# Performance work log

Hardware: AMD Instinct MI355X
Metric: run time of the kernel (lower is better)

Reference implementation:

```python
import jax, jax.numpy as jnp
import numpy as np

GAMMA = 2.5
K = 4
RHO = 0.085
TAU_CLIP = 5.0
NUM_HEADS = 8


def setup_inputs() -> dict:
    key = jax.random.key(0)
    ks = jax.random.split(key, 4)
    B, T, C = 2, 2048, 512
    x = jax.random.normal(ks[0], (B, T, C), jnp.float32)
    tau = jax.random.uniform(ks[1], (B, T, T), jnp.float32)
    s = 1.0 / np.sqrt(C)
    Wqkv = jax.random.normal(ks[2], (C, 3 * C), jnp.float32) * s
    bqkv = jnp.zeros((3 * C,), jnp.float32)
    Wproj = jax.random.normal(ks[3], (C, C), jnp.float32) * s
    bproj = jnp.zeros((C,), jnp.float32)
    return dict(x=x, tau=tau, Wqkv=Wqkv, bqkv=bqkv, Wproj=Wproj, bproj=bproj)


def reference(x, tau, Wqkv, bqkv, Wproj, bproj):
    B, T, C = x.shape
    H = NUM_HEADS
    D = C // H
    qkv = x @ Wqkv + bqkv                       # [B,T,3C]
    q, k, v = jnp.split(qkv, 3, axis=-1)
    q = q.reshape(B, T, H, D).transpose(0, 2, 1, 3)   # [B,H,T,D]
    k = k.reshape(B, T, H, D).transpose(0, 2, 1, 3)
    v = v.reshape(B, T, H, D).transpose(0, 2, 1, 3)
    scale = D ** -0.5
    logits = jnp.einsum('bhtd,bhsd->bhts', q, k) * scale   # [B,H,T,T]
    pheromone_bias = GAMMA * jnp.log(tau + 1e-8)           # [B,T,T]
    logits = logits + pheromone_bias[:, None]
    # top-K keys per query from tau define the sparse mask (LOCAL_WINDOW=0)
    k_val = min(K, T)
    idx = jax.lax.top_k(tau, k_val)[1]                     # [B,T,K]
    mask = jnp.zeros((B, T, T), bool).at[
        jnp.arange(B)[:, None, None], jnp.arange(T)[None, :, None], idx
    ].set(True)
    logits = jnp.where(mask[:, None], logits, -jnp.inf)
    attn = jax.nn.softmax(logits, axis=-1)                 # [B,H,T,T]
    # EMA pheromone (tau) update, no gradient in original (torch.no_grad)
    signal = attn.mean(axis=1)                             # [B,T,T]
    tau_new = (1.0 - RHO) * tau + signal ** 3
    tau_new = tau_new / (tau_new.sum(axis=-1, keepdims=True) + 1e-8)
    tau_new = jnp.minimum(tau_new, TAU_CLIP)
    tau_new = jax.lax.stop_gradient(tau_new)
    out = jnp.einsum('bhts,bhsd->bthd', attn, v).reshape(B, T, C)
    out = out @ Wproj + bproj
    return out, tau_new
```

## Files before the change

kernel.cpp:

```cpp
#include <hip/hip_runtime.h>
#include <hip/hip_bf16.h>
#include <math.h>

#define BB 2
#define TT 2048
#define CC 512
#define HH 8
#define DD 64
#define KK 4
#define C3 1536
#define MROWS (BB*TT)

#define G1_NT (C3/64)
#define G1_BLOCKS (G1_NT*(MROWS/128))
#define G2_NT (CC/64)
#define G2_BLOCKS (G2_NT*(MROWS/64))

typedef __attribute__((ext_vector_type(8))) short bf16x8;
typedef __attribute__((ext_vector_type(4))) float floatx4;

static __device__ __forceinline__ unsigned short f2bf(float f) {
  unsigned int u = __float_as_uint(f);
  return (unsigned short)((u + 0x7fffu + ((u >> 16) & 1u)) >> 16);
}
static __device__ __forceinline__ float bf2f(unsigned short u) {
  return __uint_as_float(((unsigned int)u) << 16);
}

static __device__ __forceinline__ int xcd_swz(int bid, int nblk) {
  const int cpx = nblk >> 3;
  return (bid & 7) * cpx + (bid >> 3);
}

template<bool BF16OUT>
static __device__ __forceinline__ void gemm_body(
    int bid, int nt,
    const unsigned short* __restrict__ A,
    const unsigned short* __restrict__ Bt,
    const float* __restrict__ bias,
    void* __restrict__ Cout, int N, int K) {
  __shared__ unsigned short As[128][64];
  __shared__ unsigned short Bs[64][64];
  const int tid  = threadIdx.x;
  const int wave = tid >> 6;
  const int lane = tid & 63;
  const int n0 = (bid % nt) * 64;
  const int m0 = (bid / nt) * 128;
  const int m_off = (wave >> 1) * 64;
  const int n_off = (wave & 1) * 32;
  const int fr = lane & 15;
  const int fq = lane >> 4;
  const int srow   = lane >> 3;
  const int schunk = ((lane & 7) ^ srow) * 8;

  floatx4 acc[4][2];
#pragma unroll
  for (int i = 0; i < 4; ++i)
#pragma unroll
    for (int j = 0; j < 2; ++j) acc[i][j] = (floatx4){0.f, 0.f, 0.f, 0.f};

  for (int k0 = 0; k0 < K; k0 += 64) {
#pragma unroll
    for (int s = 0; s < 4; ++s) {
      const int r0 = wave * 32 + s * 8;
      const unsigned short* ga = A + (size_t)(m0 + r0 + srow) * K + k0 + schunk;
      __builtin_amdgcn_global_load_lds(
          (const __attribute__((address_space(1))) void*)ga,
          (__attribute__((address_space(3))) void*)&As[r0][0], 16, 0, 0);
    }
#pragma unroll
    for (int s = 0; s < 2; ++s) {
      const int r0 = wave * 16 + s * 8;
      const unsigned short* gb = Bt + (size_t)(n0 + r0 + srow) * K + k0 + schunk;
      __builtin_amdgcn_global_load_lds(
          (const __attribute__((address_space(1))) void*)gb,
          (__attribute__((address_space(3))) void*)&Bs[r0][0], 16, 0, 0);
    }
    __syncthreads();
#pragma unroll
    for (int kk = 0; kk < 2; ++kk) {
      bf16x8 a[4], b[2];
#pragma unroll
      for (int i = 0; i < 4; ++i) {
        const int row = m_off + i * 16 + fr;
        a[i] = *(const bf16x8*)&As[row][(((kk << 2) + fq) ^ (row & 7)) * 8];
      }
#pragma unroll
      for (int j = 0; j < 2; ++j) {
        const int row = n_off + j * 16 + fr;
        b[j] = *(const bf16x8*)&Bs[row][(((kk << 2) + fq) ^ (row & 7)) * 8];
      }
#pragma unroll
      for (int i = 0; i < 4; ++i)
#pragma unroll
        for (int j = 0; j < 2; ++j)
          acc[i][j] = __builtin_amdgcn_mfma_f32_16x16x32_bf16(a[i], b[j], acc[i][j], 0, 0, 0);
    }
    __syncthreads();
  }
#pragma unroll
  for (int j = 0; j < 2; ++j) {
    int col = n0 + n_off + j * 16 + fr;
    float bv = bias[col];
#pragma unroll
    for (int i = 0; i < 4; ++i) {
#pragma unroll
      for (int r = 0; r < 4; ++r) {
        int row = m0 + m_off + i * 16 + fq * 4 + r;
        float v = acc[i][j][r] + bv;
        if (BF16OUT) ((unsigned short*)Cout)[(size_t)row * N + col] = f2bf(v);
        else         ((float*)Cout)[(size_t)row * N + col] = v;
      }
    }
  }
}

static __device__ __forceinline__ void gemm_body64(
    int bid, int nt,
    const unsigned short* __restrict__ A,
    const unsigned short* __restrict__ Bt,
    const float* __restrict__ bias,
    float* __restrict__ Cout, int N, int K) {
  __shared__ unsigned short As[64][64];
  __shared__ unsigned short Bs[64][64];
  const int tid  = threadIdx.x;
  const int wave = tid >> 6;
  const int lane = tid & 63;
  const int n0 = (bid % nt) * 64;
  const int m0 = (bid / nt) * 64;
  const int m_off = (wave >> 1) * 32;
  const int n_off = (wave & 1) * 32;
  const int fr = lane & 15;
  const int fq = lane >> 4;
  const int srow   = lane >> 3;
  const int schunk = ((lane & 7) ^ srow) * 8;

  floatx4 acc[2][2];
#pragma unroll
  for (int i = 0; i < 2; ++i)
#pragma unroll
    for (int j = 0; j < 2; ++j) acc[i][j] = (floatx4){0.f, 0.f, 0.f, 0.f};

  for (int k0 = 0; k0 < K; k0 += 64) {
#pragma unroll
    for (int s = 0; s < 2; ++s) {
      const int r0 = wave * 16 + s * 8;
      const unsigned short* ga = A + (size_t)(m0 + r0 + srow) * K + k0 + schunk;
      __builtin_amdgcn_global_load_lds(
          (const __attribute__((address_space(1))) void*)ga,
          (__attribute__((address_space(3))) void*)&As[r0][0], 16, 0, 0);
      const unsigned short* gb = Bt + (size_t)(n0 + r0 + srow) * K + k0 + schunk;
      __builtin_amdgcn_global_load_lds(
          (const __attribute__((address_space(1))) void*)gb,
          (__attribute__((address_space(3))) void*)&Bs[r0][0], 16, 0, 0);
    }
    __syncthreads();
#pragma unroll
    for (int kk = 0; kk < 2; ++kk) {
      bf16x8 a[2], b[2];
#pragma unroll
      for (int i = 0; i < 2; ++i) {
        const int row = m_off + i * 16 + fr;
        a[i] = *(const bf16x8*)&As[row][(((kk << 2) + fq) ^ (row & 7)) * 8];
      }
#pragma unroll
      for (int j = 0; j < 2; ++j) {
        const int row = n_off + j * 16 + fr;
        b[j] = *(const bf16x8*)&Bs[row][(((kk << 2) + fq) ^ (row & 7)) * 8];
      }
#pragma unroll
      for (int i = 0; i < 2; ++i)
#pragma unroll
        for (int j = 0; j < 2; ++j)
          acc[i][j] = __builtin_amdgcn_mfma_f32_16x16x32_bf16(a[i], b[j], acc[i][j], 0, 0, 0);
    }
    __syncthreads();
  }
#pragma unroll
  for (int j = 0; j < 2; ++j) {
    int col = n0 + n_off + j * 16 + fr;
    float bv = bias[col];
#pragma unroll
    for (int i = 0; i < 2; ++i) {
#pragma unroll
      for (int r = 0; r < 4; ++r) {
        int row = m0 + m_off + i * 16 + fq * 4 + r;
        Cout[(size_t)row * N + col] = acc[i][j][r] + bv;
      }
    }
  }
}

static __device__ __forceinline__ bool kv_better(float av, int ai, float bv, int bi) {
  return av > bv || (av == bv && ai < bi);
}
static __device__ __forceinline__ void kv_ce(float* v, int* i, int a, int b) {
  if (!kv_better(v[a], i[a], v[b], i[b])) {
    float tv = v[a]; v[a] = v[b]; v[b] = tv;
    int   ti = i[a]; i[a] = i[b]; i[b] = ti;
  }
}
static __device__ __forceinline__ void kv_merge(
    float* av, int* ai, const float* bv, const int* bi) {
  float cv[4]; int ci[4];
#pragma unroll
  for (int j = 0; j < 4; ++j) {
    bool t = kv_better(av[j], ai[j], bv[3 - j], bi[3 - j]);
    cv[j] = t ? av[j] : bv[3 - j];
    ci[j] = t ? ai[j] : bi[3 - j];
  }
  kv_ce(cv, ci, 0, 2); kv_ce(cv, ci, 1, 3);
  kv_ce(cv, ci, 0, 1); kv_ce(cv, ci, 2, 3);
#pragma unroll
  for (int j = 0; j < 4; ++j) { av[j] = cv[j]; ai[j] = ci[j]; }
}

static __device__ __forceinline__ void top4_local(
    const float* e, int base, float* tv, int* ti) {
  tv[0] = tv[1] = tv[2] = tv[3] = -1e30f;
  ti[0] = ti[1] = ti[2] = ti[3] = 1 << 30;
#pragma unroll
  for (int k = 0; k < 8; ++k) {
    float v = e[k];
    if (v > tv[3]) {
      tv[3] = v; ti[3] = base + k;
      if (tv[3] > tv[2]) { float a=tv[2]; tv[2]=tv[3]; tv[3]=a; int c=ti[2]; ti[2]=ti[3]; ti[3]=c; }
      if (tv[2] > tv[1]) { float a=tv[1]; tv[1]=tv[2]; tv[2]=a; int c=ti[1]; ti[1]=ti[2]; ti[2]=c; }
      if (tv[1] > tv[0]) { float a=tv[0]; tv[0]=tv[1]; tv[1]=a; int c=ti[0]; ti[0]=ti[1]; ti[1]=c; }
    }
  }
}

static __device__ __forceinline__ void merge4(
    const float sw[4][4], const int si[4][4], int* io, float* vo) {
  float m0[4], m1[4]; int x0[4], x1[4];
#pragma unroll
  for (int j = 0; j < 4; ++j) { m0[j] = sw[0][j]; x0[j] = si[0][j]; }
#pragma unroll
  for (int j = 0; j < 4; ++j) { m1[j] = sw[1][j]; x1[j] = si[1][j]; }
  kv_merge(m0, x0, m1, x1);
#pragma unroll
  for (int j = 0; j < 4; ++j) { m1[j] = sw[2][j]; x1[j] = si[2][j]; }
  float m2[4]; int x2[4];
#pragma unroll
  for (int j = 0; j < 4; ++j) { m2[j] = sw[3][j]; x2[j] = si[3][j]; }
  kv_merge(m1, x1, m2, x2);
  kv_merge(m0, x0, m1, x1);
#pragma unroll
  for (int j = 0; j < 4; ++j) { io[j] = x0[j]; vo[j] = m0[j]; }
}

static __device__ __forceinline__ void transpose_body(
    int t, int nbx, const float* __restrict__ W, unsigned short* __restrict__ Wt,
    int R, int Cn) {
  __shared__ unsigned short tile[32][33];
  const int c0 = (t % nbx) * 32, r0 = (t / nbx) * 32;
  const int tx = threadIdx.x & 31, ty = threadIdx.x >> 5;
#pragma unroll
  for (int i = 0; i < 4; ++i) {
    int r = ty + i * 8;
    tile[r][tx] = f2bf(W[(size_t)(r0 + r) * Cn + c0 + tx]);
  }
  __syncthreads();
#pragma unroll
  for (int i = 0; i < 4; ++i) {
    int r = ty + i * 8;
    Wt[(size_t)(c0 + r) * R + r0 + tx] = tile[tx][r];
  }
}

__global__ __launch_bounds__(256) void prep_kernel(
    const float* __restrict__ x, unsigned short* __restrict__ x_bf,
    const float* __restrict__ Wqkv, unsigned short* __restrict__ wqkv_t,
    const float* __restrict__ Wproj, unsigned short* __restrict__ wproj_t) {
  const int bid = blockIdx.x;
  if (bid < 1024) {
    int g = bid * 256 + threadIdx.x;
    const float4* p = (const float4*)x;
    float4 f0 = p[g * 2], f1 = p[g * 2 + 1];
    union { unsigned short u[8]; uint4 v; } pk;
    pk.u[0]=f2bf(f0.x); pk.u[1]=f2bf(f0.y); pk.u[2]=f2bf(f0.z); pk.u[3]=f2bf(f0.w);
    pk.u[4]=f2bf(f1.x); pk.u[5]=f2bf(f1.y); pk.u[6]=f2bf(f1.z); pk.u[7]=f2bf(f1.w);
    ((uint4*)x_bf)[g] = pk.v;
  } else if (bid < 1024 + 768) {
    transpose_body(bid - 1024, C3 / 32, Wqkv, wqkv_t, CC, C3);
  } else {
    transpose_body(bid - 1792, CC / 32, Wproj, wproj_t, CC, CC);
  }
}

__global__ __launch_bounds__(256) void gemm1_kernel(
    const unsigned short* __restrict__ x_bf,
    const unsigned short* __restrict__ wqkv_t,
    const float* __restrict__ bqkv, unsigned short* __restrict__ qkv_bf) {
  gemm_body<true>(xcd_swz(blockIdx.x, G1_BLOCKS), G1_NT,
                  x_bf, wqkv_t, bqkv, qkv_bf, C3, CC);
}

__global__ __launch_bounds__(256) void row2_kernel(
    const unsigned short* __restrict__ qkv, const float* __restrict__ tau,
    unsigned short* __restrict__ attn_bf, float* __restrict__ tau_out) {
  const int rowA = blockIdx.x * 2;
  const int rowB = rowA + 1;
  const int bA   = rowA >> 11;
  const int bB   = rowB >> 11;
  const int tid  = threadIdx.x;
  const int wv   = tid >> 6;
  const int lane = tid & 63;

  __shared__ int   idx4[2][KK];
  __shared__ float tau4[2][KK];
  __shared__ float ps[2][HH][KK];
  __shared__ float s3s[2][KK];
  __shared__ float swv[2][4][4];
  __shared__ int   swi[2][4][4];
  __shared__ float wsum[2][4];

  const float4* rpA = (const float4*)(tau + (size_t)rowA * TT);
  const float4* rpB = (const float4*)(tau + (size_t)rowB * TT);
  float4 a0 = rpA[tid * 2], a1 = rpA[tid * 2 + 1];
  float4 b0 = rpB[tid * 2], b1 = rpB[tid * 2 + 1];
  float qvA[2], qvB[2];
  qvA[0] = bf2f(qkv[(size_t)rowA * C3 + wv * DD + lane]);
  qvA[1] = bf2f(qkv[(size_t)rowA * C3 + (wv + 4) * DD + lane]);
  qvB[0] = bf2f(qkv[(size_t)rowB * C3 + wv * DD + lane]);
  qvB[1] = bf2f(qkv[(size_t)rowB * C3 + (wv + 4) * DD + lane]);
  float eA[8] = { a0.x, a0.y, a0.z, a0.w, a1.x, a1.y, a1.z, a1.w };
  float eB[8] = { b0.x, b0.y, b0.z, b0.w, b1.x, b1.y, b1.z, b1.w };
  const int base = tid * 8;

  float tvA[4], tvB[4]; int tiA[4], tiB[4];
  top4_local(eA, base, tvA, tiA);
  top4_local(eB, base, tvB, tiB);

#pragma unroll
  for (int step = 1; step <= 32; step <<= 1) {
    float bvA[4], bvB[4]; int biA[4], biB[4];
#pragma unroll
    for (int j = 0; j < 4; ++j) {
      bvA[j] = __shfl_xor(tvA[j], step, 64);
      biA[j] = __shfl_xor(tiA[j], step, 64);
      bvB[j] = __shfl_xor(tvB[j], step, 64);
      biB[j] = __shfl_xor(tiB[j], step, 64);
    }
    kv_merge(tvA, tiA, bvA, biA);
    kv_merge(tvB, tiB, bvB, biB);
  }
  if (lane == 0) {
#pragma unroll
    for (int j = 0; j < 4; ++j) {
      swv[0][wv][j] = tvA[j]; swi[0][wv][j] = tiA[j];
      swv[1][wv][j] = tvB[j]; swi[1][wv][j] = tiB[j];
    }
  }
  __syncthreads();
  if (tid == 0)  merge4(swv[0], swi[0], idx4[0], tau4[0]);
  if (tid == 64) merge4(swv[1], swi[1], idx4[1], tau4[1]);
  __syncthreads();

  int   i4A[KK], i4B[KK]; float t4A[KK], t4B[KK];
#pragma unroll
  for (int j = 0; j < KK; ++j) {
    i4A[j] = idx4[0][j]; t4A[j] = tau4[0][j];
    i4B[j] = idx4[1][j]; t4B[j] = tau4[1][j];
  }

#pragma unroll
  for (int hh = 0; hh < 2; ++hh) {
    const int h = wv + hh * 4;
    float kvA[KK], vvA[KK], kvB[KK], vvB[KK];
#pragma unroll
    for (int j = 0; j < KK; ++j) {
      size_t bsA = ((size_t)(bA * TT + i4A[j])) * C3 + h * DD + lane;
      size_t bsB = ((size_t)(bB * TT + i4B[j])) * C3 + h * DD + lane;
      kvA[j] = bf2f(qkv[bsA + CC]);
      vvA[j] = bf2f(qkv[bsA + 2 * CC]);
      kvB[j] = bf2f(qkv[bsB + CC]);
      vvB[j] = bf2f(qkv[bsB + 2 * CC]);
    }
    float pA[KK], pB[KK];
#pragma unroll
    for (int j = 0; j < KK; ++j) { pA[j] = qvA[hh] * kvA[j]; pB[j] = qvB[hh] * kvB[j]; }
#pragma unroll
    for (int off = 32; off > 0; off >>= 1) {
#pragma unroll
      for (int j = 0; j < KK; ++j) pA[j] += __shfl_xor(pA[j], off, 64);
#pragma unroll
      for (int j = 0; j < KK; ++j) pB[j] += __shfl_xor(pB[j], off, 64);
    }
    float lgA[KK], lgB[KK];
#pragma unroll
    for (int j = 0; j < KK; ++j) {
      lgA[j] = pA[j] * 0.125f + 2.5f * logf(t4A[j] + 1e-8f);
      lgB[j] = pB[j] * 0.125f + 2.5f * logf(t4B[j] + 1e-8f);
    }
    float mA = fmaxf(fmaxf(lgA[0], lgA[1]), fmaxf(lgA[2], lgA[3]));
    float mB = fmaxf(fmaxf(lgB[0], lgB[1]), fmaxf(lgB[2], lgB[3]));
    float dA = 0.f, dB = 0.f;
#pragma unroll
    for (int j = 0; j < KK; ++j) { pA[j] = expf(lgA[j] - mA); dA += pA[j]; }
#pragma unroll
    for (int j = 0; j < KK; ++j) { pB[j] = expf(lgB[j] - mB); dB += pB[j]; }
    float ivA = 1.f / dA, ivB = 1.f / dB;
#pragma unroll
    for (int j = 0; j < KK; ++j) { pA[j] *= ivA; pB[j] *= ivB; }
    float oA = 0.f, oB = 0.f;
#pragma unroll
    for (int j = 0; j < KK; ++j) { oA += pA[j] * vvA[j]; oB += pB[j] * vvB[j]; }
    attn_bf[(size_t)rowA * CC + h * DD + lane] = f2bf(oA);
    attn_bf[(size_t)rowB * CC + h * DD + lane] = f2bf(oB);
    if (lane < KK) { ps[0][h][lane] = pA[lane]; ps[1][h][lane] = pB[lane]; }
  }
  __syncthreads();
  if (tid < KK) {
    float s = 0.f;
#pragma unroll
    for (int k = 0; k < HH; ++k) s += ps[0][k][tid];
    s *= (1.0f / HH);
    s3s[0][tid] = s * s * s;
  } else if (tid >= 64 && tid < 64 + KK) {
    const int j = tid - 64;
    float s = 0.f;
#pragma unroll
    for (int k = 0; k < HH; ++k) s += ps[1][k][j];
    s *= (1.0f / HH);
    s3s[1][j] = s * s * s;
  }
  __syncthreads();

  float s3A[KK], s3B[KK];
#pragma unroll
  for (int j = 0; j < KK; ++j) { s3A[j] = s3s[0][j]; s3B[j] = s3s[1][j]; }
  const float keep = 1.0f - 0.085f;
  float locA = 0.f, locB = 0.f;
#pragma unroll
  for (int i = 0; i < 8; ++i) {
    float ta = keep * eA[i];
    float tb = keep * eB[i];
#pragma unroll
    for (int j = 0; j < KK; ++j) {
      if (base + i == i4A[j]) ta += s3A[j];
      if (base + i == i4B[j]) tb += s3B[j];
    }
    eA[i] = ta; locA += ta;
    eB[i] = tb; locB += tb;
  }
#pragma unroll
  for (int off = 32; off > 0; off >>= 1) {
    locA += __shfl_xor(locA, off, 64);
    locB += __shfl_xor(locB, off, 64);
  }
  if (lane == 0) { wsum[0][wv] = locA; wsum[1][wv] = locB; }
  __syncthreads();
  float totA = wsum[0][0] + wsum[0][1] + wsum[0][2] + wsum[0][3];
  float totB = wsum[1][0] + wsum[1][1] + wsum[1][2] + wsum[1][3];
  float invA = 1.f / (totA + 1e-8f);
  float invB = 1.f / (totB + 1e-8f);
  float4* opA = (float4*)(tau_out + (size_t)rowA * TT);
  float4 oa0 = { fminf(eA[0]*invA,5.f), fminf(eA[1]*invA,5.f), fminf(eA[2]*invA,5.f), fminf(eA[3]*invA,5.f) };
  float4 oa1 = { fminf(eA[4]*invA,5.f), fminf(eA[5]*invA,5.f), fminf(eA[6]*invA,5.f), fminf(eA[7]*invA,5.f) };
  opA[tid * 2] = oa0;
  opA[tid * 2 + 1] = oa1;
  float4* opB = (float4*)(tau_out + (size_t)rowB * TT);
  float4 ob0 = { fminf(eB[0]*invB,5.f), fminf(eB[1]*invB,5.f), fminf(eB[2]*invB,5.f), fminf(eB[3]*invB,5.f) };
  float4 ob1 = { fminf(eB[4]*invB,5.f), fminf(eB[5]*invB,5.f), fminf(eB[6]*invB,5.f), fminf(eB[7]*invB,5.f) };
  opB[tid * 2] = ob0;
  opB[tid * 2 + 1] = ob1;
}

__global__ __launch_bounds__(256) void gemm2_kernel(
    const unsigned short* __restrict__ attn_bf,
    const unsigned short* __restrict__ wproj_t,
    const float* __restrict__ bproj, float* __restrict__ out) {
  gemm_body64(xcd_swz(blockIdx.x, G2_BLOCKS), G2_NT,
              attn_bf, wproj_t, bproj, out, CC, CC);
}

extern "C" void kernel_launch(void* const* d_in, const int* in_sizes, int n_in,
                              void* d_out, int out_size, void* d_ws, size_t ws_size,
                              hipStream_t stream) {
  const float* x     = (const float*)d_in[0];
  const float* tau   = (const float*)d_in[1];
  const float* Wqkv  = (const float*)d_in[2];
  const float* bqkv  = (const float*)d_in[3];
  const float* Wproj = (const float*)d_in[4];
  const float* bproj = (const float*)d_in[5];

  float* out     = (float*)d_out;
  float* tau_new = out + (size_t)MROWS * CC;

  char* w = (char*)d_ws;
  unsigned short* qkv_bf  = (unsigned short*)w; w += (size_t)MROWS * C3 * 2;
  unsigned short* x_bf    = (unsigned short*)w; w += (size_t)MROWS * CC * 2;
  unsigned short* wqkv_t  = (unsigned short*)w; w += (size_t)C3 * CC * 2;
  unsigned short* wproj_t = (unsigned short*)w; w += (size_t)CC * CC * 2;
  unsigned short* attn_bf = (unsigned short*)w;

  prep_kernel<<<2048, 256, 0, stream>>>(x, x_bf, Wqkv, wqkv_t, Wproj, wproj_t);

  gemm1_kernel<<<G1_BLOCKS, 256, 0, stream>>>(x_bf, wqkv_t, bqkv, qkv_bf);

  row2_kernel<<<MROWS / 2, 256, 0, stream>>>(qkv_bf, tau, attn_bf, tau_new);

  gemm2_kernel<<<G2_BLOCKS, 256, 0, stream>>>(attn_bf, wproj_t, bproj, out);
}
```

Baseline: 142.3 us.

## Move top-4 tau selection into GEMM1 launch as extra blocks

```diff
diff --git a/kernel.cpp b/kernel.cpp
--- a/kernel.cpp
+++ b/kernel.cpp
@@ -215,10 +215,16 @@
   for (int j = 0; j < 4; ++j) { av[j] = cv[j]; ai[j] = ci[j]; }
 }
 
-static __device__ __forceinline__ void top4_local(
-    const float* e, int base, float* tv, int* ti) {
-  tv[0] = tv[1] = tv[2] = tv[3] = -1e30f;
-  ti[0] = ti[1] = ti[2] = ti[3] = 1 << 30;
+static __device__ __forceinline__ void topk_body(
+    int row, const float* __restrict__ tau, int* __restrict__ idx_out) {
+  const int tid = threadIdx.x;
+  const float4* rp = (const float4*)(tau + (size_t)row * TT);
+  float4 f0 = rp[tid * 2], f1 = rp[tid * 2 + 1];
+  float e[8] = { f0.x, f0.y, f0.z, f0.w, f1.x, f1.y, f1.z, f1.w };
+  const int base = tid * 8;
+
+  float tv[4] = { -1e30f, -1e30f, -1e30f, -1e30f };
+  int   ti[4] = { 1 << 30, 1 << 30, 1 << 30, 1 << 30 };
 #pragma unroll
   for (int k = 0; k < 8; ++k) {
     float v = e[k];
@@ -229,25 +235,41 @@
       if (tv[1] > tv[0]) { float a=tv[0]; tv[0]=tv[1]; tv[1]=a; int c=ti[0]; ti[0]=ti[1]; ti[1]=c; }
     }
   }
-}
-
-static __device__ __forceinline__ void merge4(
-    const float sw[4][4], const int si[4][4], int* io, float* vo) {
-  float m0[4], m1[4]; int x0[4], x1[4];
-#pragma unroll
-  for (int j = 0; j < 4; ++j) { m0[j] = sw[0][j]; x0[j] = si[0][j]; }
-#pragma unroll
-  for (int j = 0; j < 4; ++j) { m1[j] = sw[1][j]; x1[j] = si[1][j]; }
-  kv_merge(m0, x0, m1, x1);
-#pragma unroll
-  for (int j = 0; j < 4; ++j) { m1[j] = sw[2][j]; x1[j] = si[2][j]; }
-  float m2[4]; int x2[4];
-#pragma unroll
-  for (int j = 0; j < 4; ++j) { m2[j] = sw[3][j]; x2[j] = si[3][j]; }
-  kv_merge(m1, x1, m2, x2);
-  kv_merge(m0, x0, m1, x1);
-#pragma unroll
-  for (int j = 0; j < 4; ++j) { io[j] = x0[j]; vo[j] = m0[j]; }
+#pragma unroll
+  for (int step = 1; step <= 32; step <<= 1) {
+    float bv[4]; int bi[4];
+#pragma unroll
+    for (int j = 0; j < 4; ++j) {
+      bv[j] = __shfl_xor(tv[j], step, 64);
+      bi[j] = __shfl_xor(ti[j], step, 64);
+    }
+    kv_merge(tv, ti, bv, bi);
+  }
+  __shared__ float swv[4][4];
+  __shared__ int   swi[4][4];
+  const int wave = tid >> 6, lane = tid & 63;
+  if (lane == 0) {
+#pragma unroll
+    for (int j = 0; j < 4; ++j) { swv[wave][j] = tv[j]; swi[wave][j] = ti[j]; }
+  }
+  __syncthreads();
+  if (tid == 0) {
+    float m0[4], m1[4]; int x0[4], x1[4];
+#pragma unroll
+    for (int j = 0; j < 4; ++j) { m0[j] = swv[0][j]; x0[j] = swi[0][j]; }
+#pragma unroll
+    for (int j = 0; j < 4; ++j) { m1[j] = swv[1][j]; x1[j] = swi[1][j]; }
+    kv_merge(m0, x0, m1, x1);
+#pragma unroll
+    for (int j = 0; j < 4; ++j) { m1[j] = swv[2][j]; x1[j] = swi[2][j]; }
+    float m2[4]; int x2[4];
+#pragma unroll
+    for (int j = 0; j < 4; ++j) { m2[j] = swv[3][j]; x2[j] = swi[3][j]; }
+    kv_merge(m1, x1, m2, x2);
+    kv_merge(m0, x0, m1, x1);
+    int4 w = { x0[0], x0[1], x0[2], x0[3] };
+    *((int4*)(idx_out + row * KK)) = w;
+  }
 }
 
 static __device__ __forceinline__ void transpose_body(
@@ -289,17 +311,22 @@
   }
 }
 
-__global__ __launch_bounds__(256) void gemm1_kernel(
+__global__ __launch_bounds__(256) void gemm1_topk_kernel(
     const unsigned short* __restrict__ x_bf,
     const unsigned short* __restrict__ wqkv_t,
-    const float* __restrict__ bqkv, unsigned short* __restrict__ qkv_bf) {
-  gemm_body<true>(xcd_swz(blockIdx.x, G1_BLOCKS), G1_NT,
-                  x_bf, wqkv_t, bqkv, qkv_bf, C3, CC);
+    const float* __restrict__ bqkv, unsigned short* __restrict__ qkv_bf,
+    const float* __restrict__ tau, int* __restrict__ idx_out) {
+  if (blockIdx.x < G1_BLOCKS)
+    gemm_body<true>(xcd_swz(blockIdx.x, G1_BLOCKS), G1_NT,
+                    x_bf, wqkv_t, bqkv, qkv_bf, C3, CC);
+  else
+    topk_body(blockIdx.x - G1_BLOCKS, tau, idx_out);
 }
 
 __global__ __launch_bounds__(256) void row2_kernel(
     const unsigned short* __restrict__ qkv, const float* __restrict__ tau,
-    unsigned short* __restrict__ attn_bf, float* __restrict__ tau_out) {
+    const int* __restrict__ idx_in, unsigned short* __restrict__ attn_bf,
+    float* __restrict__ tau_out) {
   const int rowA = blockIdx.x * 2;
   const int rowB = rowA + 1;
   const int bA   = rowA >> 11;
@@ -312,10 +339,18 @@
   __shared__ float tau4[2][KK];
   __shared__ float ps[2][HH][KK];
   __shared__ float s3s[2][KK];
-  __shared__ float swv[2][4][4];
-  __shared__ int   swi[2][4][4];
   __shared__ float wsum[2][4];
 
+  if (tid < KK) {
+    int s = idx_in[rowA * KK + tid];
+    idx4[0][tid] = s;
+    tau4[0][tid] = tau[(size_t)rowA * TT + s];
+  } else if (tid >= 64 && tid < 64 + KK) {
+    const int j = tid - 64;
+    int s = idx_in[rowB * KK + j];
+    idx4[1][j] = s;
+    tau4[1][j] = tau[(size_t)rowB * TT + s];
+  }
   const float4* rpA = (const float4*)(tau + (size_t)rowA * TT);
   const float4* rpB = (const float4*)(tau + (size_t)rowB * TT);
   float4 a0 = rpA[tid * 2], a1 = rpA[tid * 2 + 1];
@@ -328,34 +363,6 @@
   float eA[8] = { a0.x, a0.y, a0.z, a0.w, a1.x, a1.y, a1.z, a1.w };
   float eB[8] = { b0.x, b0.y, b0.z, b0.w, b1.x, b1.y, b1.z, b1.w };
   const int base = tid * 8;
-
-  float tvA[4], tvB[4]; int tiA[4], tiB[4];
-  top4_local(eA, base, tvA, tiA);
-  top4_local(eB, base, tvB, tiB);
-
-#pragma unroll
-  for (int step = 1; step <= 32; step <<= 1) {
-    float bvA[4], bvB[4]; int biA[4], biB[4];
-#pragma unroll
-    for (int j = 0; j < 4; ++j) {
-      bvA[j] = __shfl_xor(tvA[j], step, 64);
-      biA[j] = __shfl_xor(tiA[j], step, 64);
-      bvB[j] = __shfl_xor(tvB[j], step, 64);
-      biB[j] = __shfl_xor(tiB[j], step, 64);
-    }
-    kv_merge(tvA, tiA, bvA, biA);
-    kv_merge(tvB, tiB, bvB, biB);
-  }
-  if (lane == 0) {
-#pragma unroll
-    for (int j = 0; j < 4; ++j) {
-      swv[0][wv][j] = tvA[j]; swi[0][wv][j] = tiA[j];
-      swv[1][wv][j] = tvB[j]; swi[1][wv][j] = tiB[j];
-    }
-  }
-  __syncthreads();
-  if (tid == 0)  merge4(swv[0], swi[0], idx4[0], tau4[0]);
-  if (tid == 64) merge4(swv[1], swi[1], idx4[1], tau4[1]);
   __syncthreads();
 
   int   i4A[KK], i4B[KK]; float t4A[KK], t4B[KK];
@@ -494,13 +501,15 @@
   unsigned short* x_bf    = (unsigned short*)w; w += (size_t)MROWS * CC * 2;
   unsigned short* wqkv_t  = (unsigned short*)w; w += (size_t)C3 * CC * 2;
   unsigned short* wproj_t = (unsigned short*)w; w += (size_t)CC * CC * 2;
-  unsigned short* attn_bf = (unsigned short*)w;
+  unsigned short* attn_bf = (unsigned short*)w; w += (size_t)MROWS * CC * 2;
+  int* idx = (int*)w;
 
   prep_kernel<<<2048, 256, 0, stream>>>(x, x_bf, Wqkv, wqkv_t, Wproj, wproj_t);
 
-  gemm1_kernel<<<G1_BLOCKS, 256, 0, stream>>>(x_bf, wqkv_t, bqkv, qkv_bf);
-
-  row2_kernel<<<MROWS / 2, 256, 0, stream>>>(qkv_bf, tau, attn_bf, tau_new);
+  gemm1_topk_kernel<<<G1_BLOCKS + MROWS, 256, 0, stream>>>(
+      x_bf, wqkv_t, bqkv, qkv_bf, tau, idx);
+
+  row2_kernel<<<MROWS / 2, 256, 0, stream>>>(qkv_bf, tau, idx, attn_bf, tau_new);
 
   gemm2_kernel<<<G2_BLOCKS, 256, 0, stream>>>(attn_bf, wproj_t, bproj, out);
 }
```

After: 145.0 us. No clear change (+1.9%).
